# Performance work log

Measured on AMD Instinct MI355X. Metric: run time of the kernel, lower is better.

## Reference

```python
import jax, jax.numpy as jnp
import numpy as np

B, S, D_IN, D_OUT, BLK = 2, 2048, 4096, 16384, 32
NBLK = D_IN // BLK  # 128


def setup_inputs() -> dict:
    key = jax.random.key(0)
    k_x, k_q, k_s, k_b = jax.random.split(key, 4)
    x = jax.random.normal(k_x, (B, S, D_IN), dtype=jnp.float32)
    # GGML Q8_0: signed 8-bit quants per block of 32
    qs = jax.random.randint(k_q, (D_OUT, NBLK, BLK), -128, 128, dtype=jnp.int32)
    # per-block scales (stand-in for the fp16 'd' field); small magnitude
    scales = jax.random.uniform(k_s, (D_OUT, NBLK), dtype=jnp.float32) * 0.02
    bias = jax.random.normal(k_b, (D_OUT,), dtype=jnp.float32)
    return {"x": x, "qs": qs, "scales": scales, "bias": bias}


def reference(x, qs, scales, bias):
    # _materialize_weight: block dequantize (d * q per block) then cast to input dtype
    # qs: [O, NBLK, BLK], scales: [O, NBLK] -> W: [O, D_IN]
    W = (scales[:, :, None] * qs.astype(x.dtype)).reshape(D_OUT, D_IN)
    # host Linear: y = x @ W^T + b
    y = jnp.einsum('bsd,od->bso', x, W) + bias
    return y
```

## Files before the change

### kernel.cpp

```cpp
#include <hip/hip_runtime.h>
#include <cstdint>
#include <cstddef>

#define M_DIM 4096
#define N_DIM 16384
#define K_DIM 4096
#define NBLK_Q 128

#define BM 256
#define BN 256
#define BK 32
#define KSTEPS (K_DIM / BK)
#define BUFB 8192
#define NBUF 4

typedef int i32x4 __attribute__((ext_vector_type(4)));
typedef int i32x16 __attribute__((ext_vector_type(16)));

#define SFENCE() __builtin_amdgcn_sched_barrier(0)
#define BAR() __builtin_amdgcn_s_barrier()
#define WAITVM(n) asm volatile("s_waitcnt vmcnt(" #n ")")
#define WAITLG0() asm volatile("s_waitcnt lgkmcnt(0)")

__global__ __launch_bounds__(256) void quant_x(const float* __restrict__ x,
                                               char* __restrict__ A8S,
                                               float* __restrict__ sxr) {
  const int m = blockIdx.x;
  const int t = threadIdx.x;
  const float* xr = x + (size_t)m * K_DIM + t * 16;
  float4 v[4];
#pragma unroll
  for (int i = 0; i < 4; ++i) v[i] = ((const float4*)xr)[i];
  float amax = 0.f;
#pragma unroll
  for (int i = 0; i < 4; ++i)
    amax = fmaxf(amax, fmaxf(fmaxf(fabsf(v[i].x), fabsf(v[i].y)),
                             fmaxf(fabsf(v[i].z), fabsf(v[i].w))));
#pragma unroll
  for (int off = 32; off; off >>= 1) amax = fmaxf(amax, __shfl_xor(amax, off, 64));
  __shared__ float wmax[4];
  if ((t & 63) == 0) wmax[t >> 6] = amax;
  __syncthreads();
  amax = fmaxf(fmaxf(wmax[0], wmax[1]), fmaxf(wmax[2], wmax[3]));
  const float inv = 127.0f / amax;
  if (t == 0) sxr[m] = amax / 127.0f;
  unsigned d[4];
#pragma unroll
  for (int i = 0; i < 4; ++i) {
    int q0 = (int)rintf(v[i].x * inv), q1 = (int)rintf(v[i].y * inv);
    int q2 = (int)rintf(v[i].z * inv), q3 = (int)rintf(v[i].w * inv);
    d[i] = (q0 & 0xff) | ((q1 & 0xff) << 8) | ((q2 & 0xff) << 16) | ((q3 & 0xff) << 24);
  }
  const int k32 = t >> 1, kg = t & 1;
  const int mtile = m >> 8, mm = m & 255, m32 = mm >> 5, r = mm & 31;
  int4* dst = (int4*)(A8S + ((size_t)(mtile * 128 + k32)) * 8192 + m32 * 1024 + kg * 512 + r * 16);
  *dst = make_int4(d[0], d[1], d[2], d[3]);
}

__global__ __launch_bounds__(256) void pack_w8(const int* __restrict__ qs,
                                               const float* __restrict__ scales,
                                               char* __restrict__ B8S,
                                               float* __restrict__ swc) {
  const int o = blockIdx.x * 4 + (threadIdx.x >> 6);
  const int l = threadIdx.x & 63;
  const float s0 = scales[(size_t)o * NBLK_Q + l];
  const float s1 = scales[(size_t)o * NBLK_Q + 64 + l];
  float S = fmaxf(s0, s1);
#pragma unroll
  for (int off = 32; off; off >>= 1) S = fmaxf(S, __shfl_xor(S, off, 64));
  if (l == 0) swc[o] = S;
  const float rS = 1.0f / S;
  const int nt = o >> 8, col = o & 255, n32 = col >> 5, c = col & 31;
#pragma unroll
  for (int h = 0; h < 2; ++h) {
    const int nb = l + 64 * h;
    const float ratio = ((h == 0) ? s0 : s1) * rS;
    const int4* q = (const int4*)(qs + ((size_t)o * NBLK_Q + nb) * 32);
    unsigned d[8];
#pragma unroll
    for (int g = 0; g < 8; ++g) {
      int4 v = q[g];
      int a0 = (int)rintf((float)v.x * ratio);
      int a1 = (int)rintf((float)v.y * ratio);
      int a2 = (int)rintf((float)v.z * ratio);
      int a3 = (int)rintf((float)v.w * ratio);
      d[g] = (a0 & 0xff) | ((a1 & 0xff) << 8) | ((a2 & 0xff) << 16) | ((a3 & 0xff) << 24);
    }
    char* dst = B8S + ((size_t)(nt * 128 + nb)) * 8192 + n32 * 1024 + c * 16;
    ((int4*)dst)[0] = make_int4(d[0], d[1], d[2], d[3]);
    ((int4*)(dst + 512))[0] = make_int4(d[4], d[5], d[6], d[7]);
  }
}

__global__ __launch_bounds__(512, 2) void gemm_i8(
    const char* __restrict__ A8S, const char* __restrict__ B8S,
    const float* __restrict__ sxr, const float* __restrict__ swc,
    const float* __restrict__ bias, float* __restrict__ C) {
  __shared__ __align__(16) char lds[NBUF * BUFB];

  const int tid = threadIdx.x;
  const int w = tid >> 6;
  const int l = tid & 63;
  const int wm = w >> 2;
  const int wn = w & 3;

  const int bid = blockIdx.x;
  const int xcd = bid & 7;
  const int k = bid >> 3;
  const int mtile = xcd * 2 + (k & 1);
  const int ntile = k >> 1;
  const int brow = mtile * BM;
  const int bcol = ntile * BN;

  const char* srcA = A8S + (size_t)mtile * 128 * 8192 + w * 1024 + l * 16;
  const char* srcBf = B8S + (size_t)ntile * 128 * 8192 + wn * 2048 + l * 16;
  const int doffA = w * 1024 + l * 16;
  const int roffA = wm * 4096 + l * 16;

  i32x16 acc[4][2] = {};
  i32x4 ca0, ca1, ca2, ca3, na0, na1, na2, na3;
  i32x4 cb0, cb1, nb0, nb1;
  int4 gaC, gaN;

  {
    int4 t0 = *(const int4*)(srcA);
    int4 t1 = *(const int4*)(srcA + 8192);
    WAITVM(0);
    *(int4*)(lds + doffA) = t0;
    *(int4*)(lds + BUFB + doffA) = t1;
    WAITLG0();
    SFENCE(); BAR(); SFENCE();
    cb0 = *(const i32x4*)(srcBf);
    cb1 = *(const i32x4*)(srcBf + 1024);
    gaC = *(const int4*)(srcA + 2 * 8192);
    ca0 = *(const i32x4*)(lds + roffA);
    ca1 = *(const i32x4*)(lds + roffA + 1024);
    ca2 = *(const i32x4*)(lds + roffA + 2048);
    ca3 = *(const i32x4*)(lds + roffA + 3072);
    WAITVM(1);
    WAITLG0();
    SFENCE();
  }

#define STEP(KT, CA0, CA1, CA2, CA3, NA0, NA1, NA2, NA3, CB0, CB1, NB0, NB1, GAC, GAN) \
  do {                                                                         \
    WAITVM(1);                  \
    const char* rb = lds + (((KT) + 1) & 3) * BUFB;                            \
    NA0 = *(const i32x4*)(rb + roffA);                                         \
    NA1 = *(const i32x4*)(rb + roffA + 1024);                                  \
    NA2 = *(const i32x4*)(rb + roffA + 2048);                                  \
    NA3 = *(const i32x4*)(rb + roffA + 3072);                                  \
    {                                                                          \
      const int qf = ((KT) + 1 > KSTEPS - 1) ? (KSTEPS - 1) : ((KT) + 1);      \
      NB0 = *(const i32x4*)(srcBf + (size_t)qf * 8192);                        \
      NB1 = *(const i32x4*)(srcBf + (size_t)qf * 8192 + 1024);                 \
      const int qa = ((KT) + 3 > KSTEPS - 1) ? (KSTEPS - 1) : ((KT) + 3);      \
      GAN = *(const int4*)(srcA + (size_t)qa * 8192);                          \
    }                                                                          \
    SFENCE();                                                                  \
    __builtin_amdgcn_s_setprio(1);                                             \
    acc[0][0] = __builtin_amdgcn_mfma_i32_32x32x32_i8(CA0, CB0, acc[0][0], 0, 0, 0); \
    acc[0][1] = __builtin_amdgcn_mfma_i32_32x32x32_i8(CA0, CB1, acc[0][1], 0, 0, 0); \
    acc[1][0] = __builtin_amdgcn_mfma_i32_32x32x32_i8(CA1, CB0, acc[1][0], 0, 0, 0); \
    acc[1][1] = __builtin_amdgcn_mfma_i32_32x32x32_i8(CA1, CB1, acc[1][1], 0, 0, 0); \
    acc[2][0] = __builtin_amdgcn_mfma_i32_32x32x32_i8(CA2, CB0, acc[2][0], 0, 0, 0); \
    acc[2][1] = __builtin_amdgcn_mfma_i32_32x32x32_i8(CA2, CB1, acc[2][1], 0, 0, 0); \
    acc[3][0] = __builtin_amdgcn_mfma_i32_32x32x32_i8(CA3, CB0, acc[3][0], 0, 0, 0); \
    acc[3][1] = __builtin_amdgcn_mfma_i32_32x32x32_i8(CA3, CB1, acc[3][1], 0, 0, 0); \
    __builtin_amdgcn_s_setprio(0);                                             \
    SFENCE();                                                                  \
    WAITVM(3);               \
    {                                                                          \
      char* wb = lds + (((KT) + 2) & 3) * BUFB;                                \
      *(int4*)(wb + doffA) = GAC;                                              \
    }                                                                          \
    SFENCE();                                                                  \
    WAITLG0();                       \
    SFENCE(); BAR(); SFENCE();                                                 \
  } while (0)

  for (int kt = 0; kt < KSTEPS; kt += 2) {
    STEP(kt, ca0, ca1, ca2, ca3, na0, na1, na2, na3, cb0, cb1, nb0, nb1, gaC, gaN);
    STEP(kt + 1, na0, na1, na2, na3, ca0, ca1, ca2, ca3, nb0, nb1, cb0, cb1, gaN, gaC);
  }
#undef STEP

#pragma unroll
  for (int i = 0; i < 4; ++i) {
    const int rbx = brow + wm * 128 + i * 32 + 4 * (l >> 5);
#pragma unroll
    for (int j = 0; j < 2; ++j) {
      const int col = bcol + wn * 64 + j * 32 + (l & 31);
      const float Sw = swc[col];
      const float bv = bias[col];
#pragma unroll
      for (int r = 0; r < 16; ++r) {
        const int row = rbx + (r & 3) + 8 * (r >> 2);
        C[(size_t)row * N_DIM + col] = (float)acc[i][j][r] * (sxr[row] * Sw) + bv;
      }
    }
  }
}

__global__ void naive_gemm(const float* __restrict__ x, const int* __restrict__ qs,
                           const float* __restrict__ scales, const float* __restrict__ bias,
                           float* __restrict__ y) {
  size_t idx = (size_t)blockIdx.x * 256 + threadIdx.x;
  if (idx >= (size_t)M_DIM * N_DIM) return;
  int o = (int)(idx % N_DIM);
  size_t m = idx / N_DIM;
  const float* xr = x + m * K_DIM;
  const int* q = qs + (size_t)o * K_DIM;
  const float* sc = scales + (size_t)o * NBLK_Q;
  float sum = 0.f;
  for (int nb = 0; nb < NBLK_Q; ++nb) {
    float s = sc[nb];
    float bs = 0.f;
#pragma unroll 8
    for (int b = 0; b < 32; ++b) bs += xr[nb * 32 + b] * (float)q[nb * 32 + b];
    sum += s * bs;
  }
  y[idx] = sum + bias[o];
}

extern "C" void kernel_launch(void* const* d_in, const int* in_sizes, int n_in,
                              void* d_out, int out_size, void* d_ws, size_t ws_size,
                              hipStream_t stream) {
  const float* x = (const float*)d_in[0];
  const int* qs = (const int*)d_in[1];
  const float* scales = (const float*)d_in[2];
  const float* bias = (const float*)d_in[3];
  float* y = (float*)d_out;

  const size_t A8_bytes = (size_t)M_DIM * K_DIM;
  const size_t B8_bytes = (size_t)N_DIM * K_DIM;
  const size_t SX_bytes = (size_t)M_DIM * 4;
  const size_t SW_bytes = (size_t)N_DIM * 4;

  if (ws_size < A8_bytes + B8_bytes + SX_bytes + SW_bytes) {
    size_t total = (size_t)M_DIM * N_DIM;
    naive_gemm<<<(unsigned)((total + 255) / 256), 256, 0, stream>>>(x, qs, scales, bias, y);
    return;
  }

  char* A8S = (char*)d_ws;
  char* B8S = A8S + A8_bytes;
  float* sxr = (float*)(B8S + B8_bytes);
  float* swc = (float*)((char*)sxr + SX_bytes);

  quant_x<<<M_DIM, 256, 0, stream>>>(x, A8S, sxr);
  pack_w8<<<N_DIM / 4, 256, 0, stream>>>(qs, scales, B8S, swc);
  gemm_i8<<<(M_DIM / BM) * (N_DIM / BN), 512, 0, stream>>>(A8S, B8S, sxr, swc, bias, y);
}
```

Before: 469.7 us.

## Stage both A and B through LDS with BK=64 double-buffered ping-pong pipeline

Restructures the int8 GEMM main loop so that both A and B tiles go through LDS. Before, only A was staged there and B fragments were read straight from global memory into registers. K tiles grow from 32 to 64 with two 32KB buffers instead of four 8KB buffers. Each tile is split into four MFMA clusters separated by barriers, with global prefetches for tile k+2 interleaved between them. The aim is shared B reuse across waves and fewer global loads per wave, at the cost of many more workgroup barriers and more LDS traffic.

```diff
diff --git a/kernel.cpp b/kernel.cpp
--- a/kernel.cpp
+++ b/kernel.cpp
@@ -9,10 +9,10 @@
 
 #define BM 256
 #define BN 256
-#define BK 32
-#define KSTEPS (K_DIM / BK)
-#define BUFB 8192
-#define NBUF 4
+#define BK 64
+#define KTILES (K_DIM / BK)
+#define BUFB 32768
+#define NBUF 2
 
 typedef int i32x4 __attribute__((ext_vector_type(4)));
 typedef int i32x16 __attribute__((ext_vector_type(16)));
@@ -113,77 +113,107 @@
   const int bcol = ntile * BN;
 
   const char* srcA = A8S + (size_t)mtile * 128 * 8192 + w * 1024 + l * 16;
-  const char* srcBf = B8S + (size_t)ntile * 128 * 8192 + wn * 2048 + l * 16;
-  const int doffA = w * 1024 + l * 16;
-  const int roffA = wm * 4096 + l * 16;
+  const char* srcB = B8S + (size_t)ntile * 128 * 8192 + w * 1024 + l * 16;
+  const int doff = w * 1024 + l * 16;
+  const int rA = wm * 4096 + l * 16;
+  const int rB = wn * 2048 + l * 16;
 
   i32x16 acc[4][2] = {};
-  i32x4 ca0, ca1, ca2, ca3, na0, na1, na2, na3;
-  i32x4 cb0, cb1, nb0, nb1;
-  int4 gaC, gaN;
+  i32x4 aa0, aa1, bb0, bb1;
+  int4 cA0, cA1, cB0, cB1;
+  int4 nA0, nA1, nB0, nB1;
 
   {
     int4 t0 = *(const int4*)(srcA);
     int4 t1 = *(const int4*)(srcA + 8192);
+    int4 t2 = *(const int4*)(srcB);
+    int4 t3 = *(const int4*)(srcB + 8192);
     WAITVM(0);
-    *(int4*)(lds + doffA) = t0;
-    *(int4*)(lds + BUFB + doffA) = t1;
+    *(int4*)(lds + doff) = t0;
+    *(int4*)(lds + 8192 + doff) = t1;
+    *(int4*)(lds + 16384 + doff) = t2;
+    *(int4*)(lds + 24576 + doff) = t3;
+    cA0 = *(const int4*)(srcA + 2 * 8192);
+    cA1 = *(const int4*)(srcA + 3 * 8192);
+    cB0 = *(const int4*)(srcB + 2 * 8192);
+    cB1 = *(const int4*)(srcB + 3 * 8192);
     WAITLG0();
     SFENCE(); BAR(); SFENCE();
-    cb0 = *(const i32x4*)(srcBf);
-    cb1 = *(const i32x4*)(srcBf + 1024);
-    gaC = *(const int4*)(srcA + 2 * 8192);
-    ca0 = *(const i32x4*)(lds + roffA);
-    ca1 = *(const i32x4*)(lds + roffA + 1024);
-    ca2 = *(const i32x4*)(lds + roffA + 2048);
-    ca3 = *(const i32x4*)(lds + roffA + 3072);
-    WAITVM(1);
-    WAITLG0();
-    SFENCE();
-  }
-
-#define STEP(KT, CA0, CA1, CA2, CA3, NA0, NA1, NA2, NA3, CB0, CB1, NB0, NB1, GAC, GAN) \
+  }
+
+#define TILE(KT, CA0, CA1, CB0, CB1, NA0, NA1, NB0, NB1)                       \
   do {                                                                         \
-    WAITVM(1);                  \
-    const char* rb = lds + (((KT) + 1) & 3) * BUFB;                            \
-    NA0 = *(const i32x4*)(rb + roffA);                                         \
-    NA1 = *(const i32x4*)(rb + roffA + 1024);                                  \
-    NA2 = *(const i32x4*)(rb + roffA + 2048);                                  \
-    NA3 = *(const i32x4*)(rb + roffA + 3072);                                  \
-    {                                                                          \
-      const int qf = ((KT) + 1 > KSTEPS - 1) ? (KSTEPS - 1) : ((KT) + 1);      \
-      NB0 = *(const i32x4*)(srcBf + (size_t)qf * 8192);                        \
-      NB1 = *(const i32x4*)(srcBf + (size_t)qf * 8192 + 1024);                 \
-      const int qa = ((KT) + 3 > KSTEPS - 1) ? (KSTEPS - 1) : ((KT) + 3);      \
-      GAN = *(const int4*)(srcA + (size_t)qa * 8192);                          \
-    }                                                                          \
+    const char* bb = lds + ((KT) & 1) * BUFB;                                  \
+    char* nb = lds + (((KT) + 1) & 1) * BUFB;                                  \
+    const int qn = ((KT) + 2 > KTILES - 1) ? (KTILES - 1) : ((KT) + 2);        \
+    const size_t gq = (size_t)qn * 16384;                                      \
+                                                           \
+    aa0 = *(const i32x4*)(bb + rA);                                            \
+    aa1 = *(const i32x4*)(bb + rA + 1024);                                     \
+    bb0 = *(const i32x4*)(bb + 16384 + rB);                                    \
+    bb1 = *(const i32x4*)(bb + 16384 + rB + 1024);                             \
+    NA0 = *(const int4*)(srcA + gq);                                           \
+    SFENCE(); BAR(); WAITLG0(); SFENCE();                                      \
+    __builtin_amdgcn_s_setprio(1);                                             \
+    acc[0][0] = __builtin_amdgcn_mfma_i32_32x32x32_i8(aa0, bb0, acc[0][0], 0, 0, 0); \
+    acc[0][1] = __builtin_amdgcn_mfma_i32_32x32x32_i8(aa0, bb1, acc[0][1], 0, 0, 0); \
+    acc[1][0] = __builtin_amdgcn_mfma_i32_32x32x32_i8(aa1, bb0, acc[1][0], 0, 0, 0); \
+    acc[1][1] = __builtin_amdgcn_mfma_i32_32x32x32_i8(aa1, bb1, acc[1][1], 0, 0, 0); \
+    __builtin_amdgcn_s_setprio(0);                                             \
+    SFENCE(); BAR(); SFENCE();                                                 \
+                                           \
+    aa0 = *(const i32x4*)(bb + rA + 2048);                                     \
+    aa1 = *(const i32x4*)(bb + rA + 3072);                                     \
+    NA1 = *(const int4*)(srcA + gq + 8192);                                    \
+    SFENCE(); BAR(); WAITLG0(); SFENCE();                                      \
+    __builtin_amdgcn_s_setprio(1);                                             \
+    acc[2][0] = __builtin_amdgcn_mfma_i32_32x32x32_i8(aa0, bb0, acc[2][0], 0, 0, 0); \
+    acc[2][1] = __builtin_amdgcn_mfma_i32_32x32x32_i8(aa0, bb1, acc[2][1], 0, 0, 0); \
+    acc[3][0] = __builtin_amdgcn_mfma_i32_32x32x32_i8(aa1, bb0, acc[3][0], 0, 0, 0); \
+    acc[3][1] = __builtin_amdgcn_mfma_i32_32x32x32_i8(aa1, bb1, acc[3][1], 0, 0, 0); \
+    __builtin_amdgcn_s_setprio(0);                                             \
+    SFENCE(); BAR(); SFENCE();                                                 \
+                                                           \
+    aa0 = *(const i32x4*)(bb + 8192 + rA);                                     \
+    aa1 = *(const i32x4*)(bb + 8192 + rA + 1024);                              \
+    bb0 = *(const i32x4*)(bb + 24576 + rB);                                    \
+    bb1 = *(const i32x4*)(bb + 24576 + rB + 1024);                             \
+    NB0 = *(const int4*)(srcB + gq);                                           \
+    SFENCE(); BAR(); WAITLG0(); SFENCE();                                      \
+    __builtin_amdgcn_s_setprio(1);                                             \
+    acc[0][0] = __builtin_amdgcn_mfma_i32_32x32x32_i8(aa0, bb0, acc[0][0], 0, 0, 0); \
+    acc[0][1] = __builtin_amdgcn_mfma_i32_32x32x32_i8(aa0, bb1, acc[0][1], 0, 0, 0); \
+    acc[1][0] = __builtin_amdgcn_mfma_i32_32x32x32_i8(aa1, bb0, acc[1][0], 0, 0, 0); \
+    acc[1][1] = __builtin_amdgcn_mfma_i32_32x32x32_i8(aa1, bb1, acc[1][1], 0, 0, 0); \
+    __builtin_amdgcn_s_setprio(0);                                             \
+    SFENCE(); BAR(); SFENCE();                                                 \
+                             \
+    aa0 = *(const i32x4*)(bb + 8192 + rA + 2048);                              \
+    aa1 = *(const i32x4*)(bb + 8192 + rA + 3072);                              \
+    NB1 = *(const int4*)(srcB + gq + 8192);                                    \
+    SFENCE(); BAR(); WAITLG0(); SFENCE();                                      \
+    __builtin_amdgcn_s_setprio(1);                                             \
+    acc[2][0] = __builtin_amdgcn_mfma_i32_32x32x32_i8(aa0, bb0, acc[2][0], 0, 0, 0); \
+    acc[2][1] = __builtin_amdgcn_mfma_i32_32x32x32_i8(aa0, bb1, acc[2][1], 0, 0, 0); \
+    acc[3][0] = __builtin_amdgcn_mfma_i32_32x32x32_i8(aa1, bb0, acc[3][0], 0, 0, 0); \
+    acc[3][1] = __builtin_amdgcn_mfma_i32_32x32x32_i8(aa1, bb1, acc[3][1], 0, 0, 0); \
+    __builtin_amdgcn_s_setprio(0);                                             \
     SFENCE();                                                                  \
-    __builtin_amdgcn_s_setprio(1);                                             \
-    acc[0][0] = __builtin_amdgcn_mfma_i32_32x32x32_i8(CA0, CB0, acc[0][0], 0, 0, 0); \
-    acc[0][1] = __builtin_amdgcn_mfma_i32_32x32x32_i8(CA0, CB1, acc[0][1], 0, 0, 0); \
-    acc[1][0] = __builtin_amdgcn_mfma_i32_32x32x32_i8(CA1, CB0, acc[1][0], 0, 0, 0); \
-    acc[1][1] = __builtin_amdgcn_mfma_i32_32x32x32_i8(CA1, CB1, acc[1][1], 0, 0, 0); \
-    acc[2][0] = __builtin_amdgcn_mfma_i32_32x32x32_i8(CA2, CB0, acc[2][0], 0, 0, 0); \
-    acc[2][1] = __builtin_amdgcn_mfma_i32_32x32x32_i8(CA2, CB1, acc[2][1], 0, 0, 0); \
-    acc[3][0] = __builtin_amdgcn_mfma_i32_32x32x32_i8(CA3, CB0, acc[3][0], 0, 0, 0); \
-    acc[3][1] = __builtin_amdgcn_mfma_i32_32x32x32_i8(CA3, CB1, acc[3][1], 0, 0, 0); \
-    __builtin_amdgcn_s_setprio(0);                                             \
+    WAITVM(4);                \
+    *(int4*)(nb + doff) = CA0;                                                 \
+    *(int4*)(nb + 8192 + doff) = CA1;                                          \
+    *(int4*)(nb + 16384 + doff) = CB0;                                         \
+    *(int4*)(nb + 24576 + doff) = CB1;                                         \
     SFENCE();                                                                  \
-    WAITVM(3);               \
-    {                                                                          \
-      char* wb = lds + (((KT) + 2) & 3) * BUFB;                                \
-      *(int4*)(wb + doffA) = GAC;                                              \
-    }                                                                          \
-    SFENCE();                                                                  \
-    WAITLG0();                       \
+    WAITLG0();                                                                 \
     SFENCE(); BAR(); SFENCE();                                                 \
   } while (0)
 
-  for (int kt = 0; kt < KSTEPS; kt += 2) {
-    STEP(kt, ca0, ca1, ca2, ca3, na0, na1, na2, na3, cb0, cb1, nb0, nb1, gaC, gaN);
-    STEP(kt + 1, na0, na1, na2, na3, ca0, ca1, ca2, ca3, nb0, nb1, cb0, cb1, gaN, gaC);
-  }
-#undef STEP
+  for (int kt = 0; kt < KTILES; kt += 2) {
+    TILE(kt, cA0, cA1, cB0, cB1, nA0, nA1, nB0, nB1);
+    TILE(kt + 1, nA0, nA1, nB0, nB1, cA0, cA1, cB0, cB1);
+  }
+#undef TILE
 
 #pragma unroll
   for (int i = 0; i < 4; ++i) {
```

After: 425.6 us. 9.4% less time.

## Shrink GEMM tiles to 128x128 with BK 64 and double-buffered LDS

Applied to the files above, without the earlier changes.

Restructures the int8 GEMM from 256x256 tiles with 512 threads, BK=32 and four LDS buffers to 128x128 tiles with 256 threads, BK=64 and two LDS buffers. Each wave now computes a 64x64 sub-tile, and the block-to-tile mapping and prefetch distances are adjusted to match. The aim is more resident blocks per CU and fewer barriers per unit of K. The cost is lower operand reuse per tile, so global traffic for both A and B roughly doubles.

```diff
diff --git a/kernel.cpp b/kernel.cpp
--- a/kernel.cpp
+++ b/kernel.cpp
@@ -7,12 +7,12 @@
 #define K_DIM 4096
 #define NBLK_Q 128
 
-#define BM 256
-#define BN 256
-#define BK 32
-#define KSTEPS (K_DIM / BK)
+#define BM 128
+#define BN 128
+#define BK 64
+#define KTILES (K_DIM / BK)
 #define BUFB 8192
-#define NBUF 4
+#define NBUF 2
 
 typedef int i32x4 __attribute__((ext_vector_type(4)));
 typedef int i32x16 __attribute__((ext_vector_type(16)));
@@ -92,7 +92,7 @@
   }
 }
 
-__global__ __launch_bounds__(512, 2) void gemm_i8(
+__global__ __launch_bounds__(256, 3) void gemm_i8(
     const char* __restrict__ A8S, const char* __restrict__ B8S,
     const float* __restrict__ sxr, const float* __restrict__ swc,
     const float* __restrict__ bias, float* __restrict__ C) {
@@ -101,96 +101,104 @@
   const int tid = threadIdx.x;
   const int w = tid >> 6;
   const int l = tid & 63;
-  const int wm = w >> 2;
-  const int wn = w & 3;
+  const int wm = w >> 1;
+  const int wn = w & 1;
 
   const int bid = blockIdx.x;
   const int xcd = bid & 7;
-  const int k = bid >> 3;
-  const int mtile = xcd * 2 + (k & 1);
-  const int ntile = k >> 1;
-  const int brow = mtile * BM;
-  const int bcol = ntile * BN;
-
-  const char* srcA = A8S + (size_t)mtile * 128 * 8192 + w * 1024 + l * 16;
-  const char* srcBf = B8S + (size_t)ntile * 128 * 8192 + wn * 2048 + l * 16;
-  const int doffA = w * 1024 + l * 16;
-  const int roffA = wm * 4096 + l * 16;
-
-  i32x16 acc[4][2] = {};
-  i32x4 ca0, ca1, ca2, ca3, na0, na1, na2, na3;
-  i32x4 cb0, cb1, nb0, nb1;
-  int4 gaC, gaN;
+  const int kk = bid >> 3;
+  const int mt = xcd * 4 + (kk & 3);
+  const int nt = kk >> 2;
+  const int brow = mt * BM;
+
+  const char* srcA = A8S + (size_t)(mt >> 1) * 1048576 + (size_t)(mt & 1) * 4096
+                     + w * 1024 + l * 16;
+  const char* srcB0 = B8S + (size_t)(nt >> 1) * 1048576
+                      + (size_t)((nt & 1) * 4 + wn * 2) * 1024 + l * 16;
+  const char* srcB1 = srcB0 + 1024;
+  const int doff = w * 1024 + l * 16;
+  const int rA = (wm * 2) * 1024 + l * 16;
+
+  i32x16 acc[2][2] = {};
+  i32x4 aa00, aa01, aa10, aa11;
+  i32x4 bc00, bc01, bc10, bc11;
+  i32x4 bn00, bn01, bn10, bn11;
+  i32x4 aC0, aC1, aN0, aN1;
 
   {
-    int4 t0 = *(const int4*)(srcA);
-    int4 t1 = *(const int4*)(srcA + 8192);
+    aN0 = *(const i32x4*)(srcA);
+    aN1 = *(const i32x4*)(srcA + 8192);
     WAITVM(0);
-    *(int4*)(lds + doffA) = t0;
-    *(int4*)(lds + BUFB + doffA) = t1;
+    *(i32x4*)(lds + doff) = aN0;
+    *(i32x4*)(lds + 4096 + doff) = aN1;
+    bc00 = *(const i32x4*)(srcB0);
+    bc01 = *(const i32x4*)(srcB1);
+    bc10 = *(const i32x4*)(srcB0 + 8192);
+    bc11 = *(const i32x4*)(srcB1 + 8192);
+    aC0 = *(const i32x4*)(srcA + 2 * 8192);
+    aC1 = *(const i32x4*)(srcA + 3 * 8192);
     WAITLG0();
     SFENCE(); BAR(); SFENCE();
-    cb0 = *(const i32x4*)(srcBf);
-    cb1 = *(const i32x4*)(srcBf + 1024);
-    gaC = *(const int4*)(srcA + 2 * 8192);
-    ca0 = *(const i32x4*)(lds + roffA);
-    ca1 = *(const i32x4*)(lds + roffA + 1024);
-    ca2 = *(const i32x4*)(lds + roffA + 2048);
-    ca3 = *(const i32x4*)(lds + roffA + 3072);
-    WAITVM(1);
-    WAITLG0();
-    SFENCE();
-  }
-
-#define STEP(KT, CA0, CA1, CA2, CA3, NA0, NA1, NA2, NA3, CB0, CB1, NB0, NB1, GAC, GAN) \
+  }
+
+#define TILE(KT, BC00, BC01, BC10, BC11, BN00, BN01, BN10, BN11, AC0, AC1, AN0, AN1) \
   do {                                                                         \
-    WAITVM(1);                  \
-    const char* rb = lds + (((KT) + 1) & 3) * BUFB;                            \
-    NA0 = *(const i32x4*)(rb + roffA);                                         \
-    NA1 = *(const i32x4*)(rb + roffA + 1024);                                  \
-    NA2 = *(const i32x4*)(rb + roffA + 2048);                                  \
-    NA3 = *(const i32x4*)(rb + roffA + 3072);                                  \
+    WAITVM(2);                              \
+    const char* bb = lds + ((KT) & 1) * BUFB;                                  \
+    aa00 = *(const i32x4*)(bb + rA);                                           \
+    aa01 = *(const i32x4*)(bb + rA + 1024);                                    \
+    aa10 = *(const i32x4*)(bb + 4096 + rA);                                    \
+    aa11 = *(const i32x4*)(bb + 4096 + rA + 1024);                             \
     {                                                                          \
-      const int qf = ((KT) + 1 > KSTEPS - 1) ? (KSTEPS - 1) : ((KT) + 1);      \
-      NB0 = *(const i32x4*)(srcBf + (size_t)qf * 8192);                        \
-      NB1 = *(const i32x4*)(srcBf + (size_t)qf * 8192 + 1024);                 \
-      const int qa = ((KT) + 3 > KSTEPS - 1) ? (KSTEPS - 1) : ((KT) + 3);      \
-      GAN = *(const int4*)(srcA + (size_t)qa * 8192);                          \
+      const int qb = ((KT) + 1 > KTILES - 1) ? (KTILES - 1) : ((KT) + 1);      \
+      const size_t ob = (size_t)qb * 16384;                                    \
+      BN00 = *(const i32x4*)(srcB0 + ob);                                      \
+      BN01 = *(const i32x4*)(srcB1 + ob);                                      \
+      BN10 = *(const i32x4*)(srcB0 + ob + 8192);                               \
+      BN11 = *(const i32x4*)(srcB1 + ob + 8192);                               \
+      const int qa = ((KT) + 2 > KTILES - 1) ? (KTILES - 1) : ((KT) + 2);      \
+      AN0 = *(const i32x4*)(srcA + (size_t)qa * 16384);                        \
+      AN1 = *(const i32x4*)(srcA + (size_t)qa * 16384 + 8192);                 \
+    }                                                                          \
+    WAITLG0();                                              \
+    SFENCE();                                                                  \
+    __builtin_amdgcn_s_setprio(1);                                             \
+    acc[0][0] = __builtin_amdgcn_mfma_i32_32x32x32_i8(aa00, BC00, acc[0][0], 0, 0, 0); \
+    acc[0][1] = __builtin_amdgcn_mfma_i32_32x32x32_i8(aa00, BC01, acc[0][1], 0, 0, 0); \
+    acc[1][0] = __builtin_amdgcn_mfma_i32_32x32x32_i8(aa01, BC00, acc[1][0], 0, 0, 0); \
+    acc[1][1] = __builtin_amdgcn_mfma_i32_32x32x32_i8(aa01, BC01, acc[1][1], 0, 0, 0); \
+    acc[0][0] = __builtin_amdgcn_mfma_i32_32x32x32_i8(aa10, BC10, acc[0][0], 0, 0, 0); \
+    acc[0][1] = __builtin_amdgcn_mfma_i32_32x32x32_i8(aa10, BC11, acc[0][1], 0, 0, 0); \
+    acc[1][0] = __builtin_amdgcn_mfma_i32_32x32x32_i8(aa11, BC10, acc[1][0], 0, 0, 0); \
+    acc[1][1] = __builtin_amdgcn_mfma_i32_32x32x32_i8(aa11, BC11, acc[1][1], 0, 0, 0); \
+    __builtin_amdgcn_s_setprio(0);                                             \
+    SFENCE();                                                                  \
+    WAITVM(6);             \
+    {                                                                          \
+      char* nb = lds + (((KT) + 1) & 1) * BUFB;                                \
+      *(i32x4*)(nb + doff) = AC0;                                              \
+      *(i32x4*)(nb + 4096 + doff) = AC1;                                       \
     }                                                                          \
     SFENCE();                                                                  \
-    __builtin_amdgcn_s_setprio(1);                                             \
-    acc[0][0] = __builtin_amdgcn_mfma_i32_32x32x32_i8(CA0, CB0, acc[0][0], 0, 0, 0); \
-    acc[0][1] = __builtin_amdgcn_mfma_i32_32x32x32_i8(CA0, CB1, acc[0][1], 0, 0, 0); \
-    acc[1][0] = __builtin_amdgcn_mfma_i32_32x32x32_i8(CA1, CB0, acc[1][0], 0, 0, 0); \
-    acc[1][1] = __builtin_amdgcn_mfma_i32_32x32x32_i8(CA1, CB1, acc[1][1], 0, 0, 0); \
-    acc[2][0] = __builtin_amdgcn_mfma_i32_32x32x32_i8(CA2, CB0, acc[2][0], 0, 0, 0); \
-    acc[2][1] = __builtin_amdgcn_mfma_i32_32x32x32_i8(CA2, CB1, acc[2][1], 0, 0, 0); \
-    acc[3][0] = __builtin_amdgcn_mfma_i32_32x32x32_i8(CA3, CB0, acc[3][0], 0, 0, 0); \
-    acc[3][1] = __builtin_amdgcn_mfma_i32_32x32x32_i8(CA3, CB1, acc[3][1], 0, 0, 0); \
-    __builtin_amdgcn_s_setprio(0);                                             \
-    SFENCE();                                                                  \
-    WAITVM(3);               \
-    {                                                                          \
-      char* wb = lds + (((KT) + 2) & 3) * BUFB;                                \
-      *(int4*)(wb + doffA) = GAC;                                              \
-    }                                                                          \
-    SFENCE();                                                                  \
-    WAITLG0();                       \
+    WAITLG0();                                                                 \
     SFENCE(); BAR(); SFENCE();                                                 \
   } while (0)
 
-  for (int kt = 0; kt < KSTEPS; kt += 2) {
-    STEP(kt, ca0, ca1, ca2, ca3, na0, na1, na2, na3, cb0, cb1, nb0, nb1, gaC, gaN);
-    STEP(kt + 1, na0, na1, na2, na3, ca0, ca1, ca2, ca3, nb0, nb1, cb0, cb1, gaN, gaC);
-  }
-#undef STEP
-
-#pragma unroll
-  for (int i = 0; i < 4; ++i) {
-    const int rbx = brow + wm * 128 + i * 32 + 4 * (l >> 5);
+  for (int kt = 0; kt < KTILES; kt += 2) {
+    TILE(kt, bc00, bc01, bc10, bc11, bn00, bn01, bn10, bn11, aC0, aC1, aN0, aN1);
+    TILE(kt + 1, bn00, bn01, bn10, bn11, bc00, bc01, bc10, bc11, aN0, aN1, aC0, aC1);
+  }
+#undef TILE
+
+  WAITVM(0);
+  SFENCE();
+
+#pragma unroll
+  for (int i = 0; i < 2; ++i) {
+    const int rbx = brow + wm * 64 + i * 32 + 4 * (l >> 5);
 #pragma unroll
     for (int j = 0; j < 2; ++j) {
-      const int col = bcol + wn * 64 + j * 32 + (l & 31);
+      const int col = nt * 128 + (wn * 2 + j) * 32 + (l & 31);
       const float Sw = swc[col];
       const float bv = bias[col];
 #pragma unroll
@@ -250,5 +258,5 @@
 
   quant_x<<<M_DIM, 256, 0, stream>>>(x, A8S, sxr);
   pack_w8<<<N_DIM / 4, 256, 0, stream>>>(qs, scales, B8S, swc);
-  gemm_i8<<<(M_DIM / BM) * (N_DIM / BN), 512, 0, stream>>>(A8S, B8S, sxr, swc, bias, y);
-}
+  gemm_i8<<<(M_DIM / BM) * (N_DIM / BN), 256, 0, stream>>>(A8S, B8S, sxr, swc, bias, y);
+}
```

Result: slower. 493.4 us (+5.0%).

## Load A fragments directly from global into registers, dropping LDS staging and barriers

Applied to the files above, without the earlier changes.

The int8 GEMM no longer stages A tiles through a 4-buffer LDS ring with per-step barriers. Each wave now loads its own A and B fragments straight from global memory into registers, double-buffered across two register sets, and waits on vmcnt only. This removes LDS traffic and the workgroup barrier every k-step. In exchange, the four waves that share A rows each fetch the same A data separately, so global and L2 traffic for A goes up several times.

```diff
diff --git a/kernel.cpp b/kernel.cpp
--- a/kernel.cpp
+++ b/kernel.cpp
@@ -11,16 +11,12 @@
 #define BN 256
 #define BK 32
 #define KSTEPS (K_DIM / BK)
-#define BUFB 8192
-#define NBUF 4
 
 typedef int i32x4 __attribute__((ext_vector_type(4)));
 typedef int i32x16 __attribute__((ext_vector_type(16)));
 
 #define SFENCE() __builtin_amdgcn_sched_barrier(0)
-#define BAR() __builtin_amdgcn_s_barrier()
 #define WAITVM(n) asm volatile("s_waitcnt vmcnt(" #n ")")
-#define WAITLG0() asm volatile("s_waitcnt lgkmcnt(0)")
 
 __global__ __launch_bounds__(256) void quant_x(const float* __restrict__ x,
                                                char* __restrict__ A8S,
@@ -96,8 +92,6 @@
     const char* __restrict__ A8S, const char* __restrict__ B8S,
     const float* __restrict__ sxr, const float* __restrict__ swc,
     const float* __restrict__ bias, float* __restrict__ C) {
-  __shared__ __align__(16) char lds[NBUF * BUFB];
-
   const int tid = threadIdx.x;
   const int w = tid >> 6;
   const int l = tid & 63;
@@ -112,78 +106,66 @@
   const int brow = mtile * BM;
   const int bcol = ntile * BN;
 
-  const char* srcA = A8S + (size_t)mtile * 128 * 8192 + w * 1024 + l * 16;
-  const char* srcBf = B8S + (size_t)ntile * 128 * 8192 + wn * 2048 + l * 16;
-  const int doffA = w * 1024 + l * 16;
-  const int roffA = wm * 4096 + l * 16;
+  const char* pA = A8S + (size_t)mtile * 1048576 + wm * 4096 + l * 16;
+  const char* pB = B8S + (size_t)ntile * 1048576 + wn * 2048 + l * 16;
 
   i32x16 acc[4][2] = {};
-  i32x4 ca0, ca1, ca2, ca3, na0, na1, na2, na3;
-  i32x4 cb0, cb1, nb0, nb1;
-  int4 gaC, gaN;
-
-  {
-    int4 t0 = *(const int4*)(srcA);
-    int4 t1 = *(const int4*)(srcA + 8192);
-    WAITVM(0);
-    *(int4*)(lds + doffA) = t0;
-    *(int4*)(lds + BUFB + doffA) = t1;
-    WAITLG0();
-    SFENCE(); BAR(); SFENCE();
-    cb0 = *(const i32x4*)(srcBf);
-    cb1 = *(const i32x4*)(srcBf + 1024);
-    gaC = *(const int4*)(srcA + 2 * 8192);
-    ca0 = *(const i32x4*)(lds + roffA);
-    ca1 = *(const i32x4*)(lds + roffA + 1024);
-    ca2 = *(const i32x4*)(lds + roffA + 2048);
-    ca3 = *(const i32x4*)(lds + roffA + 3072);
-    WAITVM(1);
-    WAITLG0();
-    SFENCE();
-  }
-
-#define STEP(KT, CA0, CA1, CA2, CA3, NA0, NA1, NA2, NA3, CB0, CB1, NB0, NB1, GAC, GAN) \
+  i32x4 xa0, xa1, xa2, xa3, xb0, xb1;
+  i32x4 ya0, ya1, ya2, ya3, yb0, yb1;
+
+  xa0 = *(const i32x4*)(pA);
+  xa1 = *(const i32x4*)(pA + 1024);
+  xa2 = *(const i32x4*)(pA + 2048);
+  xa3 = *(const i32x4*)(pA + 3072);
+  xb0 = *(const i32x4*)(pB);
+  xb1 = *(const i32x4*)(pB + 1024);
+  ya0 = *(const i32x4*)(pA + 8192);
+  ya1 = *(const i32x4*)(pA + 8192 + 1024);
+  ya2 = *(const i32x4*)(pA + 8192 + 2048);
+  ya3 = *(const i32x4*)(pA + 8192 + 3072);
+  yb0 = *(const i32x4*)(pB + 8192);
+  yb1 = *(const i32x4*)(pB + 8192 + 1024);
+  pA += 2 * 8192;
+  pB += 2 * 8192;
+
+#define STEP(KT, A0, A1, A2, A3, B0, B1)                                       \
   do {                                                                         \
-    WAITVM(1);                  \
-    const char* rb = lds + (((KT) + 1) & 3) * BUFB;                            \
-    NA0 = *(const i32x4*)(rb + roffA);                                         \
-    NA1 = *(const i32x4*)(rb + roffA + 1024);                                  \
-    NA2 = *(const i32x4*)(rb + roffA + 2048);                                  \
-    NA3 = *(const i32x4*)(rb + roffA + 3072);                                  \
+    WAITVM(6);                        \
+    SFENCE();                                                                  \
+    __builtin_amdgcn_s_setprio(1);                                             \
+    acc[0][0] = __builtin_amdgcn_mfma_i32_32x32x32_i8(A0, B0, acc[0][0], 0, 0, 0); \
+    acc[0][1] = __builtin_amdgcn_mfma_i32_32x32x32_i8(A0, B1, acc[0][1], 0, 0, 0); \
+    acc[1][0] = __builtin_amdgcn_mfma_i32_32x32x32_i8(A1, B0, acc[1][0], 0, 0, 0); \
+    acc[1][1] = __builtin_amdgcn_mfma_i32_32x32x32_i8(A1, B1, acc[1][1], 0, 0, 0); \
+    acc[2][0] = __builtin_amdgcn_mfma_i32_32x32x32_i8(A2, B0, acc[2][0], 0, 0, 0); \
+    acc[2][1] = __builtin_amdgcn_mfma_i32_32x32x32_i8(A2, B1, acc[2][1], 0, 0, 0); \
+    acc[3][0] = __builtin_amdgcn_mfma_i32_32x32x32_i8(A3, B0, acc[3][0], 0, 0, 0); \
+    acc[3][1] = __builtin_amdgcn_mfma_i32_32x32x32_i8(A3, B1, acc[3][1], 0, 0, 0); \
+    __builtin_amdgcn_s_setprio(0);                                             \
+    SFENCE();                                                                  \
+    \
+    A0 = *(const i32x4*)(pA);                                                  \
+    A1 = *(const i32x4*)(pA + 1024);                                           \
+    A2 = *(const i32x4*)(pA + 2048);                                           \
+    A3 = *(const i32x4*)(pA + 3072);                                           \
+    B0 = *(const i32x4*)(pB);                                                  \
+    B1 = *(const i32x4*)(pB + 1024);                                           \
     {                                                                          \
-      const int qf = ((KT) + 1 > KSTEPS - 1) ? (KSTEPS - 1) : ((KT) + 1);      \
-      NB0 = *(const i32x4*)(srcBf + (size_t)qf * 8192);                        \
-      NB1 = *(const i32x4*)(srcBf + (size_t)qf * 8192 + 1024);                 \
-      const int qa = ((KT) + 3 > KSTEPS - 1) ? (KSTEPS - 1) : ((KT) + 3);      \
-      GAN = *(const int4*)(srcA + (size_t)qa * 8192);                          \
+      const int adv = ((KT) + 3 <= KSTEPS - 1) ? 8192 : 0;                     \
+      pA += adv;                                                               \
+      pB += adv;                                                               \
     }                                                                          \
     SFENCE();                                                                  \
-    __builtin_amdgcn_s_setprio(1);                                             \
-    acc[0][0] = __builtin_amdgcn_mfma_i32_32x32x32_i8(CA0, CB0, acc[0][0], 0, 0, 0); \
-    acc[0][1] = __builtin_amdgcn_mfma_i32_32x32x32_i8(CA0, CB1, acc[0][1], 0, 0, 0); \
-    acc[1][0] = __builtin_amdgcn_mfma_i32_32x32x32_i8(CA1, CB0, acc[1][0], 0, 0, 0); \
-    acc[1][1] = __builtin_amdgcn_mfma_i32_32x32x32_i8(CA1, CB1, acc[1][1], 0, 0, 0); \
-    acc[2][0] = __builtin_amdgcn_mfma_i32_32x32x32_i8(CA2, CB0, acc[2][0], 0, 0, 0); \
-    acc[2][1] = __builtin_amdgcn_mfma_i32_32x32x32_i8(CA2, CB1, acc[2][1], 0, 0, 0); \
-    acc[3][0] = __builtin_amdgcn_mfma_i32_32x32x32_i8(CA3, CB0, acc[3][0], 0, 0, 0); \
-    acc[3][1] = __builtin_amdgcn_mfma_i32_32x32x32_i8(CA3, CB1, acc[3][1], 0, 0, 0); \
-    __builtin_amdgcn_s_setprio(0);                                             \
-    SFENCE();                                                                  \
-    WAITVM(3);               \
-    {                                                                          \
-      char* wb = lds + (((KT) + 2) & 3) * BUFB;                                \
-      *(int4*)(wb + doffA) = GAC;                                              \
-    }                                                                          \
-    SFENCE();                                                                  \
-    WAITLG0();                       \
-    SFENCE(); BAR(); SFENCE();                                                 \
   } while (0)
 
   for (int kt = 0; kt < KSTEPS; kt += 2) {
-    STEP(kt, ca0, ca1, ca2, ca3, na0, na1, na2, na3, cb0, cb1, nb0, nb1, gaC, gaN);
-    STEP(kt + 1, na0, na1, na2, na3, ca0, ca1, ca2, ca3, nb0, nb1, cb0, cb1, gaN, gaC);
+    STEP(kt, xa0, xa1, xa2, xa3, xb0, xb1);
+    STEP(kt + 1, ya0, ya1, ya2, ya3, yb0, yb1);
   }
 #undef STEP
+
+  WAITVM(0);
+  SFENCE();
 
 #pragma unroll
   for (int i = 0; i < 4; ++i) {
```

New measurement: 459.8 us. -2.1%, faster.
